# Optimization experiments

Measured on AMD Instinct MI355X. Metric: run time of the kernel, lower is better.

Reference implementation:

```python
import jax, jax.numpy as jnp
import numpy as np

C = 10  # cluster gap window; repo-level global constant in the original code


def _per_neuron(v, label):
    """Faithful vectorized translation of the per-(batch,neuron) Python loops.

    v:     [T] membrane potential trace
    label: scalar int target cluster count
    Returns (loss_contribution, num_cluster).
    """
    T = v.shape[0]
    t = jnp.arange(T, dtype=jnp.int32)
    spk = v >= 0.0                                   # spike positions (v >= 0)
    # exclusive prefix counts of spikes: csp[i] = #spikes in v[:i]
    csp = jnp.concatenate([jnp.zeros(1, jnp.int32), jnp.cumsum(spk.astype(jnp.int32))])
    lo = jnp.clip(t - C, 0, T)
    # a spike starts a new cluster iff no spike in the preceding C steps
    cnt_prev = csp[t] - csp[lo]
    is_start = spk & (cnt_prev == 0)
    num_cluster = jnp.sum(is_start.astype(jnp.int32))
    vmax = jnp.max(v)

    # ---- excess branch (label > num_cluster) ----
    # mask[t] = 1 iff some spike lies in [t-C, t+C]  (union of [first-C, last+C] per cluster)
    hi = jnp.clip(t + C + 1, 0, T)
    mask = (csp[hi] - csp[lo]) > 0
    full0 = jnp.all(mask)
    NEG = jnp.asarray(-1e30, v.dtype)
    m0 = jnp.max(jnp.where(mask, NEG, v))            # max over unmasked times (iter 0)
    tm = jnp.argmax(v)                               # original uses global argmax of v
    win = (t >= tm - C // 2) & (t <= tm + C // 2)
    mask2 = mask | win                               # mask after first loop iteration (fixed thereafter)
    full2 = jnp.all(mask2)
    # if mask2 full, remaining iterations pick a spike value (random in original; spikes have v>=0,
    # we use the deterministic surrogate vmax which is always a spike value when spikes exist)
    m_rest = jnp.where(full2, vmax, jnp.max(jnp.where(mask2, NEG, v)))
    label_f = label.astype(v.dtype)
    ncf = num_cluster.astype(v.dtype)
    dE = jnp.maximum(label_f - ncf, 1.0)             # safe denominator (branch-gated below)
    mean_excess = (m0 + (dE - 1.0) * m_rest) / dE
    excess_loss = jnp.where(full0, vmax, -mean_excess)

    # ---- deficit branch (label < num_cluster) ----
    BIG = T + 2 * C + 2
    lt = jax.lax.cummax(jnp.where(spk, t, -BIG))                 # nearest spike <= t
    rt = jax.lax.cummin(jnp.where(spk, t, BIG)[::-1])[::-1]      # nearest spike >= t
    in_span = (rt - lt) <= C                                     # t inside [first,last] of a cluster
    cid = jnp.cumsum(is_start.astype(jnp.int32)) - 1             # cluster id at time t
    K = T // (C + 1) + 1                                         # max possible clusters
    seg = jnp.where(in_span, cid, K)
    rec = jax.ops.segment_max(v, seg, num_segments=K + 1)[:K]    # per-cluster span max
    POS = jnp.asarray(1e30, v.dtype)
    rec = jnp.where(jnp.arange(K) < num_cluster, rec, POS)
    rec = jnp.sort(rec)                                          # ascending, real clusters first
    dD = jnp.maximum(ncf - label_f, 1.0)
    deficit_loss = jnp.sum(jnp.where(jnp.arange(K) < (num_cluster - label), rec, 0.0)) / dD

    contrib = jnp.where(label > num_cluster, excess_loss,
                        jnp.where(label < num_cluster, deficit_loss, 0.0))
    return contrib, num_cluster


def setup_inputs() -> dict:
    key = jax.random.key(0)
    k1, k2, k3 = jax.random.split(key, 3)
    B, T, N = 256, 500, 128
    vmem = jax.random.normal(k1, (B, T, N), dtype=jnp.float32)
    vlastmem = jax.random.normal(k2, (B, T, N), dtype=jnp.float32)
    labels_t = jax.random.randint(k3, (B, N), 0, 5, dtype=jnp.int32)
    return {"vmem": vmem, "vlastmem": vlastmem, "labels_t": labels_t, "ratio": 1}


def reference(vmem, vlastmem, labels_t, ratio):
    # vlastmem and ratio are unused in the original forward; kept for signature fidelity.
    vv = jnp.transpose(vmem, (0, 2, 1))  # [B, N, T]
    contrib, nclus = jax.vmap(jax.vmap(_per_neuron))(vv, labels_t)
    loss = jnp.sum(contrib)
    spike_output = nclus.astype(jnp.float32)  # [B, N] cluster counts
    return loss, spike_output
```

## Files before the change

### kernel.cpp

```cpp
#include <hip/hip_runtime.h>

namespace {
constexpr int CC    = 10;
constexpr int TT    = 500;
constexpr int NN    = 128;
constexpr int G     = 10;
constexpr int LSEG  = TT / G;
constexpr int HALO  = CC;
constexpr int ROWS  = LSEG + 2 * HALO;
constexpr int CHR   = 16;
constexpr int NSLOT = 10;
constexpr int MAXG  = TT / (CC + 1) + 1;
}

__global__ void zero_loss_kernel(float* out) {
    if (threadIdx.x == 0) out[0] = 0.0f;
}

__global__ __launch_bounds__(128)
void seg_scan_kernel(const float* __restrict__ vmem, float* __restrict__ ws) {
    const int s   = blockIdx.x;
    const int b   = blockIdx.y;
    const int tid = threadIdx.x;
    const int a   = s * LSEG;
    const int lo  = a - HALO;
    const float* __restrict__ base = vmem + (size_t)b * TT * NN;
    float* __restrict__ wsl = ws + ((size_t)(b * G + s) * NSLOT) * NN + tid;

    __shared__ __align__(16) float buf[2][CHR * NN];

    float4 ra[4], rb[4];

    auto issue = [&](int c, float4 (&r)[4]) {
        #pragma unroll
        for (int i = 0; i < 4; ++i) {
            const int f = tid + 128 * i;
            int row = lo + c * CHR + (f >> 5);
            row = row < 0 ? 0 : (row > TT - 1 ? TT - 1 : row);
            r[i] = *((const float4*)(base + (size_t)row * NN) + (f & 31));
        }
    };
    auto commit = [&](int c, const float4 (&r)[4]) {
        float4* d = (float4*)buf[c & 1];
        #pragma unroll
        for (int i = 0; i < 4; ++i) d[tid + 128 * i] = r[i];
    };

    int   ls = -(1 << 20), lcount = 0, hdne = 0, tmn = 0, hasu = 0;
    float ccm = -1e30f, rmax = -1e30f, hdm = -1e30f, vmx = -1e30f, m0 = -1e30f;
    float ring[10];

    auto scanChunk = [&](int c) {
        const float* bsrc = buf[c & 1];
        #pragma unroll
        for (int j = 0; j < CHR; ++j) {
            const int r = c * CHR + j;
            if (r >= ROWS) continue;
            const int ofs = r - HALO;
            const int t   = a + ofs;
            float v = bsrc[j * NN + tid];
            if (ofs < 0 && s == 0) v = -1.0f;
            if (ofs >= LSEG && s == G - 1) v = -1.0f;
            const bool spike = v >= 0.0f;
            if (ofs >= 0 && ofs < LSEG) {
                const float rm2 = fmaxf(rmax, v);
                if (spike) {
                    if (t - ls > CC) {
                        if (lcount > 0) wsl[(size_t)(lcount - 1) * NN] = ccm;
                        ccm = v; ++lcount;
                    } else if (lcount == 0) { hdne = 1; hdm = fmaxf(hdm, rm2); }
                    else ccm = fmaxf(ccm, rm2);
                    rmax = -1e30f;
                } else rmax = rm2;
                if (v > vmx) { vmx = v; tmn = t; }
            }
            if (spike) ls = t;
            if (r >= 2 * HALO) {
                const float vu = ring[r % 10];
                if (ls < t - 2 * CC) { hasu = 1; if (vu > m0) m0 = vu; }
            }
            ring[r % 10] = v;
        }
    };

    issue(0, ra); commit(0, ra);
    issue(1, rb);
    __syncthreads();
    scanChunk(0);
    commit(1, rb); __syncthreads();
    issue(2, ra);
    scanChunk(1);
    commit(2, ra); __syncthreads();
    issue(3, rb);
    scanChunk(2);
    commit(3, rb); __syncthreads();
    issue(4, ra);
    scanChunk(3);
    commit(4, ra); __syncthreads();
    scanChunk(4);

    if (lcount > 0) wsl[(size_t)(lcount - 1) * NN] = ccm;
    const int packed = lcount | (hdne << 3) | (hasu << 4) | (tmn << 5);
    wsl[5 * NN] = __int_as_float(packed);
    wsl[6 * NN] = hdm;
    wsl[7 * NN] = rmax;
    wsl[8 * NN] = vmx;
    wsl[9 * NN] = m0;
}

__global__ __launch_bounds__(128)
void merge_kernel(const float* __restrict__ vmem, const float* __restrict__ ws,
                  const int* __restrict__ labels, float* __restrict__ out) {
    const int b = blockIdx.x; const int tid = threadIdx.x;
    __shared__ float gl[MAXG * NN];
    __shared__ float redbuf[2];
    const float* __restrict__ col = vmem + (size_t)b * TT * NN + tid;

    int g_nc = 0, g_hasu = 0, g_tm = 0;
    float g_vmax = -1e30f, g_m0 = -1e30f;
    int g = 0; bool open = false; float cur = -1e30f, ptg = -1e30f;

    #pragma unroll
    for (int s2 = 0; s2 < G; ++s2) {
        const float* wsl = ws + ((size_t)(b * G + s2) * NSLOT) * NN + tid;
        const int packed = __float_as_int(wsl[5 * NN]);
        const int k = packed & 7, hne = (packed >> 3) & 1, hu = (packed >> 4) & 1;
        const int tms = packed >> 5;
        const float hdm = wsl[6 * NN], tg = wsl[7 * NN];
        const float vmx = wsl[8 * NN], m0s = wsl[9 * NN];
        g_nc += k; g_hasu |= hu;
        if (vmx > g_vmax) { g_vmax = vmx; g_tm = tms; }
        if (m0s > g_m0) g_m0 = m0s;
        if (open) {
            if (hne) { cur = fmaxf(cur, fmaxf(ptg, hdm)); ptg = tg; }
            if (k > 0 || !hne) { gl[g * NN + tid] = cur; ++g; open = false; }
        }
        if (k > 0) {
            for (int i = 0; i < k - 1; ++i) { gl[g * NN + tid] = wsl[(size_t)i * NN]; ++g; }
            cur = wsl[(size_t)(k - 1) * NN];
            open = true; ptg = tg;
        }
    }
    if (open) { gl[g * NN + tid] = cur; ++g; }

    const int label = labels[b * NN + tid];
    float contrib = 0.0f;
    if (label > g_nc) {
        if (!g_hasu) {
            contrib = g_vmax;
        } else {
            float mrest = g_vmax;
            const bool need2 = (label - g_nc >= 2);
            if (__any((int)need2)) {
                if (need2) {
                    const int wlo = g_tm - CC / 2, whi = g_tm + CC / 2;
                    int ls2 = -(1 << 20); float m2 = -1e30f; int has2 = 0;
                    for (int c = 0; c < TT / CC + 1; ++c) {
                        float cv[CC], pv[CC];
                        #pragma unroll
                        for (int j = 0; j < CC; ++j) {
                            const int t = c * CC + j;
                            cv[j] = (t < TT) ? col[(size_t)t * NN] : -1.0f;
                        }
                        #pragma unroll
                        for (int j = 0; j < CC; ++j) {
                            const int u = c * CC + j - CC;
                            pv[j] = (u >= 0 && u < TT) ? col[(size_t)u * NN] : -1.0f;
                        }
                        #pragma unroll
                        for (int j = 0; j < CC; ++j) {
                            const int t = c * CC + j;
                            if (cv[j] >= 0.0f) ls2 = t;
                            const int u = t - CC;
                            if (u >= 0 && u < TT) {
                                if (ls2 < t - 2 * CC && (u < wlo || u > whi)) {
                                    has2 = 1; if (pv[j] > m2) m2 = pv[j];
                                }
                            }
                        }
                    }
                    if (has2) mrest = m2;
                }
            }
            const float dE = (float)(label - g_nc);
            contrib = -((g_m0 + (dE - 1.0f) * mrest) / dE);
        }
    } else if (label < g_nc) {
        const int kk = g_nc - label;
        float ssum = 0.0f;
        for (int i = 0; i < kk; ++i) {
            float mn = 1e30f; int mj = 0;
            for (int jj = 0; jj < g_nc; ++jj) {
                const float x = gl[jj * NN + tid];
                if (x < mn) { mn = x; mj = jj; }
            }
            ssum += mn; gl[mj * NN + tid] = 1e30f;
        }
        contrib = ssum / (float)kk;
    }

    out[1 + b * NN + tid] = (float)g_nc;

    float w = contrib;
    #pragma unroll
    for (int off = 32; off > 0; off >>= 1) w += __shfl_down(w, off, 64);
    if ((tid & 63) == 0) redbuf[tid >> 6] = w;
    __syncthreads();
    if (tid == 0) atomicAdd(out, redbuf[0] + redbuf[1]);
}

extern "C" void kernel_launch(void* const* d_in, const int* in_sizes, int n_in,
                              void* d_out, int out_size, void* d_ws, size_t ws_size,
                              hipStream_t stream) {
    const float* vmem   = (const float*)d_in[0];
    const int*   labels = (const int*)d_in[2];
    float*       out    = (float*)d_out;
    float*       ws     = (float*)d_ws;

    const int B = in_sizes[2] / NN;

    hipLaunchKernelGGL(zero_loss_kernel, dim3(1), dim3(64), 0, stream, out);
    hipLaunchKernelGGL(seg_scan_kernel, dim3(G, B), dim3(NN), 0, stream, vmem, ws);
    hipLaunchKernelGGL(merge_kernel, dim3(B), dim3(NN), 0, stream, vmem, ws, labels, out);
}
```

Baseline: 199.9 us.

## Single-shot segment load, staged cluster writes, and wave-cooperative rescan in merge

The segment scan now loads all 72 rows at once into shared memory instead of double-buffering chunks. It reads the halo lookback directly from shared memory rather than a register ring, and it stages per-cluster maxima in shared memory for coalesced workspace writes. In the merge kernel, workspace values are preloaded into registers. The per-lane serial 500-step rescan for the second excess iteration is replaced by a ballot loop in which the whole wave cooperatively loads one neuron's column into shared memory and scans it in parallel, with a shuffle reduction. The zero kernel becomes a memset and launch bounds add an occupancy hint; the cost is larger register arrays and a serialized loop over the neurons that need the rescan.

```diff
diff --git a/kernel.cpp b/kernel.cpp
--- a/kernel.cpp
+++ b/kernel.cpp
@@ -7,99 +7,71 @@
 constexpr int G     = 10;
 constexpr int LSEG  = TT / G;
 constexpr int HALO  = CC;
-constexpr int ROWS  = LSEG + 2 * HALO;
-constexpr int CHR   = 16;
+constexpr int LROWS = 72;
+constexpr int NF4   = (LROWS * NN / 4) / NN;
 constexpr int NSLOT = 10;
 constexpr int MAXG  = TT / (CC + 1) + 1;
 }
 
-__global__ void zero_loss_kernel(float* out) {
-    if (threadIdx.x == 0) out[0] = 0.0f;
-}
-
-__global__ __launch_bounds__(128)
+__global__ __launch_bounds__(128, 2)
 void seg_scan_kernel(const float* __restrict__ vmem, float* __restrict__ ws) {
     const int s   = blockIdx.x;
     const int b   = blockIdx.y;
     const int tid = threadIdx.x;
     const int a   = s * LSEG;
-    const int lo  = a - HALO;
-    const float* __restrict__ base = vmem + (size_t)b * TT * NN;
-    float* __restrict__ wsl = ws + ((size_t)(b * G + s) * NSLOT) * NN + tid;
-
-    __shared__ __align__(16) float buf[2][CHR * NN];
-
-    float4 ra[4], rb[4];
-
-    auto issue = [&](int c, float4 (&r)[4]) {
-        #pragma unroll
-        for (int i = 0; i < 4; ++i) {
-            const int f = tid + 128 * i;
-            int row = lo + c * CHR + (f >> 5);
-            row = row < 0 ? 0 : (row > TT - 1 ? TT - 1 : row);
-            r[i] = *((const float4*)(base + (size_t)row * NN) + (f & 31));
-        }
-    };
-    auto commit = [&](int c, const float4 (&r)[4]) {
-        float4* d = (float4*)buf[c & 1];
-        #pragma unroll
-        for (int i = 0; i < 4; ++i) d[tid + 128 * i] = r[i];
-    };
+    int ldstart = a - HALO;
+    ldstart = ldstart < 0 ? 0 : ldstart;
+    ldstart = ldstart > TT - LROWS ? TT - LROWS : ldstart;
+    const int shift = a - ldstart;
+
+    __shared__ __align__(16) float buf[LROWS * NN];
+    __shared__ float stg[5 * NN];
+
+    const float4* __restrict__ g4 =
+        (const float4*)(vmem + ((size_t)b * TT + ldstart) * NN);
+    float4 r[NF4];
+    #pragma unroll
+    for (int i = 0; i < NF4; ++i) r[i] = g4[tid + NN * i];
+    #pragma unroll
+    for (int i = 0; i < 5; ++i) stg[i * NN + tid] = 0.0f;
+    float4* l4 = (float4*)buf;
+    #pragma unroll
+    for (int i = 0; i < NF4; ++i) l4[tid + NN * i] = r[i];
+    __syncthreads();
 
     int   ls = -(1 << 20), lcount = 0, hdne = 0, tmn = 0, hasu = 0;
     float ccm = -1e30f, rmax = -1e30f, hdm = -1e30f, vmx = -1e30f, m0 = -1e30f;
-    float ring[10];
-
-    auto scanChunk = [&](int c) {
-        const float* bsrc = buf[c & 1];
-        #pragma unroll
-        for (int j = 0; j < CHR; ++j) {
-            const int r = c * CHR + j;
-            if (r >= ROWS) continue;
-            const int ofs = r - HALO;
-            const int t   = a + ofs;
-            float v = bsrc[j * NN + tid];
-            if (ofs < 0 && s == 0) v = -1.0f;
-            if (ofs >= LSEG && s == G - 1) v = -1.0f;
-            const bool spike = v >= 0.0f;
-            if (ofs >= 0 && ofs < LSEG) {
-                const float rm2 = fmaxf(rmax, v);
-                if (spike) {
-                    if (t - ls > CC) {
-                        if (lcount > 0) wsl[(size_t)(lcount - 1) * NN] = ccm;
-                        ccm = v; ++lcount;
-                    } else if (lcount == 0) { hdne = 1; hdm = fmaxf(hdm, rm2); }
-                    else ccm = fmaxf(ccm, rm2);
-                    rmax = -1e30f;
-                } else rmax = rm2;
-                if (v > vmx) { vmx = v; tmn = t; }
-            }
-            if (spike) ls = t;
-            if (r >= 2 * HALO) {
-                const float vu = ring[r % 10];
-                if (ls < t - 2 * CC) { hasu = 1; if (vu > m0) m0 = vu; }
-            }
-            ring[r % 10] = v;
-        }
-    };
-
-    issue(0, ra); commit(0, ra);
-    issue(1, rb);
-    __syncthreads();
-    scanChunk(0);
-    commit(1, rb); __syncthreads();
-    issue(2, ra);
-    scanChunk(1);
-    commit(2, ra); __syncthreads();
-    issue(3, rb);
-    scanChunk(2);
-    commit(3, rb); __syncthreads();
-    issue(4, ra);
-    scanChunk(3);
-    commit(4, ra); __syncthreads();
-    scanChunk(4);
-
-    if (lcount > 0) wsl[(size_t)(lcount - 1) * NN] = ccm;
+    const bool firstSeg = (s == 0), lastSeg = (s == G - 1);
+
+    #pragma unroll
+    for (int ofs = -HALO; ofs < LSEG + HALO; ++ofs) {
+        const int t = a + ofs;
+        const bool invalid = (firstSeg && ofs < 0) || (lastSeg && ofs >= LSEG);
+        const float v = invalid ? -1.0f : buf[(ofs + shift) * NN + tid];
+        const bool spike = v >= 0.0f;
+        if (ofs >= 0 && ofs < LSEG) {
+            const float rm2 = fmaxf(rmax, v);
+            if (spike) {
+                if (t - ls > CC) {
+                    if (lcount > 0) stg[(lcount - 1) * NN + tid] = ccm;
+                    ccm = v; ++lcount;
+                } else if (lcount == 0) { hdne = 1; hdm = fmaxf(hdm, rm2); }
+                else ccm = fmaxf(ccm, rm2);
+                rmax = -1e30f;
+            } else rmax = rm2;
+            if (v > vmx) { vmx = v; tmn = t; }
+        }
+        if (spike) ls = t;
+        if (ofs >= HALO) {
+            const float vu = buf[(ofs - HALO + shift) * NN + tid];
+            if (ls < t - 2 * CC) { hasu = 1; if (vu > m0) m0 = vu; }
+        }
+    }
+    if (lcount > 0) stg[(lcount - 1) * NN + tid] = ccm;
+
+    float* __restrict__ wsl = ws + (size_t)(b * G + s) * NSLOT * NN + tid;
+    #pragma unroll
+    for (int i = 0; i < 5; ++i) wsl[i * NN] = stg[i * NN + tid];
     const int packed = lcount | (hdne << 3) | (hasu << 4) | (tmn << 5);
     wsl[5 * NN] = __int_as_float(packed);
     wsl[6 * NN] = hdm;
@@ -108,80 +80,103 @@
     wsl[9 * NN] = m0;
 }
 
-__global__ __launch_bounds__(128)
+__global__ __launch_bounds__(128, 2)
 void merge_kernel(const float* __restrict__ vmem, const float* __restrict__ ws,
                   const int* __restrict__ labels, float* __restrict__ out) {
-    const int b = blockIdx.x; const int tid = threadIdx.x;
+    const int b = blockIdx.x, tid = threadIdx.x, lane = tid & 63;
     __shared__ float gl[MAXG * NN];
-    __shared__ float redbuf[2];
-    const float* __restrict__ col = vmem + (size_t)b * TT * NN + tid;
-
-    int g_nc = 0, g_hasu = 0, g_tm = 0;
+    __shared__ float wbuf[2][512];
+    __shared__ float red[2];
+
+    float cm[G][5], hd[G], tg[G], vx[G], mm[G]; int pk[G];
+    const float* __restrict__ wsb = ws + (size_t)b * G * NSLOT * NN + tid;
+    #pragma unroll
+    for (int s2 = 0; s2 < G; ++s2) {
+        const float* p = wsb + (size_t)s2 * NSLOT * NN;
+        #pragma unroll
+        for (int i = 0; i < 5; ++i) cm[s2][i] = p[i * NN];
+        pk[s2] = __float_as_int(p[5 * NN]);
+        hd[s2] = p[6 * NN];
+        tg[s2] = p[7 * NN];
+        vx[s2] = p[8 * NN];
+        mm[s2] = p[9 * NN];
+    }
+
+    int g = 0, g_nc = 0, g_hasu = 0, g_tm = 0;
+    bool open = false; float cur = -1e30f, ptg = -1e30f;
     float g_vmax = -1e30f, g_m0 = -1e30f;
-    int g = 0; bool open = false; float cur = -1e30f, ptg = -1e30f;
-
     #pragma unroll
     for (int s2 = 0; s2 < G; ++s2) {
-        const float* wsl = ws + ((size_t)(b * G + s2) * NSLOT) * NN + tid;
-        const int packed = __float_as_int(wsl[5 * NN]);
-        const int k = packed & 7, hne = (packed >> 3) & 1, hu = (packed >> 4) & 1;
-        const int tms = packed >> 5;
-        const float hdm = wsl[6 * NN], tg = wsl[7 * NN];
-        const float vmx = wsl[8 * NN], m0s = wsl[9 * NN];
-        g_nc += k; g_hasu |= hu;
-        if (vmx > g_vmax) { g_vmax = vmx; g_tm = tms; }
-        if (m0s > g_m0) g_m0 = m0s;
+        const int k   = pk[s2] & 7;
+        const int hne = (pk[s2] >> 3) & 1;
+        g_nc += k; g_hasu |= (pk[s2] >> 4) & 1;
+        if (vx[s2] > g_vmax) { g_vmax = vx[s2]; g_tm = pk[s2] >> 5; }
+        if (mm[s2] > g_m0) g_m0 = mm[s2];
         if (open) {
-            if (hne) { cur = fmaxf(cur, fmaxf(ptg, hdm)); ptg = tg; }
+            if (hne) { cur = fmaxf(cur, fmaxf(ptg, hd[s2])); ptg = tg[s2]; }
             if (k > 0 || !hne) { gl[g * NN + tid] = cur; ++g; open = false; }
         }
         if (k > 0) {
-            for (int i = 0; i < k - 1; ++i) { gl[g * NN + tid] = wsl[(size_t)i * NN]; ++g; }
-            cur = wsl[(size_t)(k - 1) * NN];
-            open = true; ptg = tg;
+            #pragma unroll
+            for (int i = 0; i < 4; ++i)
+                if (i < k - 1) { gl[g * NN + tid] = cm[s2][i]; ++g; }
+            float last = cm[s2][4];
+            if (k == 1) last = cm[s2][0];
+            else if (k == 2) last = cm[s2][1];
+            else if (k == 3) last = cm[s2][2];
+            else if (k == 4) last = cm[s2][3];
+            cur = last; open = true; ptg = tg[s2];
         }
     }
     if (open) { gl[g * NN + tid] = cur; ++g; }
 
     const int label = labels[b * NN + tid];
+
+    const bool need2 = (label > g_nc) && g_hasu && (label - g_nc >= 2);
+    float mrest = g_vmax;
+    unsigned long long bal = __ballot(need2);
+    if (bal) {
+        float* wb = wbuf[tid >> 6];
+        const float* colbase = vmem + (size_t)b * TT * NN;
+        while (bal) {
+            const int f = __ffsll((unsigned long long)bal) - 1;
+            bal &= bal - 1;
+            const int   nf    = (tid & 64) | f;
+            const int   tmf   = __shfl(g_tm, f);
+            const float vmaxf = __shfl(g_vmax, f);
+            #pragma unroll
+            for (int j = 0; j < 8; ++j) {
+                const int t = lane * 8 + j;
+                wb[t] = (t < TT) ? colbase[(size_t)t * NN + nf] : -1.0f;
+            }
+            __threadfence_block();
+            int ls2 = -1000, lh = 0; float lm = -1e30f;
+            const int u0 = lane * 8;
+            for (int t2 = u0 - 10; t2 < u0 + 18; ++t2) {
+                const float v = (t2 >= 0 && t2 < 512) ? wb[t2] : -1.0f;
+                if (v >= 0.0f) ls2 = t2;
+                const int u = t2 - 10;
+                if (u >= u0 && u < u0 + 8 && u < TT) {
+                    if (ls2 < u - 10 && (u < tmf - CC / 2 || u > tmf + CC / 2)) {
+                        lh = 1; const float vu = wb[u]; if (vu > lm) lm = vu;
+                    }
+                }
+            }
+            #pragma unroll
+            for (int off = 32; off > 0; off >>= 1) {
+                lm = fmaxf(lm, __shfl_down(lm, off));
+                lh |= __shfl_down(lh, off);
+            }
+            const float res = __shfl(lh ? lm : vmaxf, 0);
+            if (lane == f) mrest = res;
+            __threadfence_block();
+        }
+    }
+
     float contrib = 0.0f;
     if (label > g_nc) {
-        if (!g_hasu) {
-            contrib = g_vmax;
-        } else {
-            float mrest = g_vmax;
-            const bool need2 = (label - g_nc >= 2);
-            if (__any((int)need2)) {
-                if (need2) {
-                    const int wlo = g_tm - CC / 2, whi = g_tm + CC / 2;
-                    int ls2 = -(1 << 20); float m2 = -1e30f; int has2 = 0;
-                    for (int c = 0; c < TT / CC + 1; ++c) {
-                        float cv[CC], pv[CC];
-                        #pragma unroll
-                        for (int j = 0; j < CC; ++j) {
-                            const int t = c * CC + j;
-                            cv[j] = (t < TT) ? col[(size_t)t * NN] : -1.0f;
-                        }
-                        #pragma unroll
-                        for (int j = 0; j < CC; ++j) {
-                            const int u = c * CC + j - CC;
-                            pv[j] = (u >= 0 && u < TT) ? col[(size_t)u * NN] : -1.0f;
-                        }
-                        #pragma unroll
-                        for (int j = 0; j < CC; ++j) {
-                            const int t = c * CC + j;
-                            if (cv[j] >= 0.0f) ls2 = t;
-                            const int u = t - CC;
-                            if (u >= 0 && u < TT) {
-                                if (ls2 < t - 2 * CC && (u < wlo || u > whi)) {
-                                    has2 = 1; if (pv[j] > m2) m2 = pv[j];
-                                }
-                            }
-                        }
-                    }
-                    if (has2) mrest = m2;
-                }
-            }
+        if (!g_hasu) contrib = g_vmax;
+        else {
             const float dE = (float)(label - g_nc);
             contrib = -((g_m0 + (dE - 1.0f) * mrest) / dE);
         }
@@ -203,10 +198,10 @@
 
     float w = contrib;
     #pragma unroll
-    for (int off = 32; off > 0; off >>= 1) w += __shfl_down(w, off, 64);
-    if ((tid & 63) == 0) redbuf[tid >> 6] = w;
+    for (int off = 32; off > 0; off >>= 1) w += __shfl_down(w, off);
+    if (lane == 0) red[tid >> 6] = w;
     __syncthreads();
-    if (tid == 0) atomicAdd(out, redbuf[0] + redbuf[1]);
+    if (tid == 0) atomicAdd(out, red[0] + red[1]);
 }
 
 extern "C" void kernel_launch(void* const* d_in, const int* in_sizes, int n_in,
@@ -219,7 +214,7 @@
 
     const int B = in_sizes[2] / NN;
 
-    hipLaunchKernelGGL(zero_loss_kernel, dim3(1), dim3(64), 0, stream, out);
+    hipMemsetAsync(out, 0, sizeof(float), stream);
     hipLaunchKernelGGL(seg_scan_kernel, dim3(G, B), dim3(NN), 0, stream, vmem, ws);
     hipLaunchKernelGGL(merge_kernel, dim3(B), dim3(NN), 0, stream, vmem, ws, labels, out);
 }
```

After: 172.5 us. 13.7% less time.
